# Kernel tuning notes

Hardware: AMD Instinct MI355X
Metric: run time of the kernel (lower is better)

The kernel has to match this reference:

```python
import jax, jax.numpy as jnp
import numpy as np

EPS = 1e-5  # torch LayerNorm default eps
DIM = 2
FEED = 10


def layernorm(x, g, b):
    mu = jnp.mean(x, axis=-1, keepdims=True)
    var = jnp.mean((x - mu) ** 2, axis=-1, keepdims=True)
    return (x - mu) * jax.lax.rsqrt(var + EPS) * g + b


def mha(q, k, v, w_in, b_in, w_out, b_out):
    # nn.MultiheadAttention with n_heads=1: head_dim == embed_dim
    E = q.shape[-1]
    wq, wk, wv = jnp.split(w_in, 3, axis=0)
    bq, bk, bv = jnp.split(b_in, 3)
    qh = q @ wq.T + bq  # [B,Sq,E]
    kh = k @ wk.T + bk  # [B,Sk,E]
    vh = v @ wv.T + bv
    scale = 1.0 / np.sqrt(E).astype(np.float32)
    scores = jnp.einsum('bqd,bkd->bqk', qh, kh) * scale  # [B,Sq,Sk]
    attn = jax.nn.softmax(scores, axis=-1)
    out = jnp.einsum('bqk,bkd->bqd', attn, vh)
    return out @ w_out.T + b_out


def setup_inputs() -> dict:
    key = jax.random.key(0)
    ks = jax.random.split(key, 16)
    d, fd = DIM, FEED
    s = 0.5
    inp = {
        'x': jax.random.normal(ks[0], (32, 32, 256, d), dtype=jnp.float32),
        'm': jax.random.normal(ks[1], (1024, 256, d), dtype=jnp.float32),
        # self-attention params
        'sa_w_in': jax.random.normal(ks[2], (3 * d, d), dtype=jnp.float32) * s,
        'sa_b_in': jnp.zeros((3 * d,), dtype=jnp.float32),
        'sa_w_out': jax.random.normal(ks[3], (d, d), dtype=jnp.float32) * s,
        'sa_b_out': jnp.zeros((d,), dtype=jnp.float32),
        # cross-attention params
        'ca_w_in': jax.random.normal(ks[4], (3 * d, d), dtype=jnp.float32) * s,
        'ca_b_in': jnp.zeros((3 * d,), dtype=jnp.float32),
        'ca_w_out': jax.random.normal(ks[5], (d, d), dtype=jnp.float32) * s,
        'ca_b_out': jnp.zeros((d,), dtype=jnp.float32),
        # layernorms
        'ln1_g': jnp.ones((d,), dtype=jnp.float32),
        'ln1_b': jnp.zeros((d,), dtype=jnp.float32),
        'ln2_g': jnp.ones((d,), dtype=jnp.float32),
        'ln2_b': jnp.zeros((d,), dtype=jnp.float32),
        'ln3_g': jnp.ones((d,), dtype=jnp.float32),
        'ln3_b': jnp.zeros((d,), dtype=jnp.float32),
        # feed-forward: Linear(d,fd) -> LayerNorm(fd) -> ReLU -> Linear(fd,d)
        'f_w1': jax.random.normal(ks[6], (fd, d), dtype=jnp.float32) * s,
        'f_b1': jnp.zeros((fd,), dtype=jnp.float32),
        'f_ln_g': jnp.ones((fd,), dtype=jnp.float32),
        'f_ln_b': jnp.zeros((fd,), dtype=jnp.float32),
        'f_w2': jax.random.normal(ks[7], (d, fd), dtype=jnp.float32) * s,
        'f_b2': jnp.zeros((d,), dtype=jnp.float32),
    }
    return inp


def reference(x, m, sa_w_in, sa_b_in, sa_w_out, sa_b_out,
              ca_w_in, ca_b_in, ca_w_out, ca_b_out,
              ln1_g, ln1_b, ln2_g, ln2_b, ln3_g, ln3_b,
              f_w1, f_b1, f_ln_g, f_ln_b, f_w2, f_b2):
    b, k, s, f = x.shape
    h = x.reshape(-1, s, f)  # [b*k, s, f]
    h = layernorm(h, ln1_g, ln1_b)
    h = h + mha(h, h, h, sa_w_in, sa_b_in, sa_w_out, sa_b_out)
    h = layernorm(h, ln2_g, ln2_b)
    h = h + mha(h, m, m, ca_w_in, ca_b_in, ca_w_out, ca_b_out)
    h = layernorm(h, ln3_g, ln3_b)
    ff = h @ f_w1.T + f_b1
    ff = layernorm(ff, f_ln_g, f_ln_b)
    ff = jax.nn.relu(ff) @ f_w2.T + f_b2
    h = h + ff
    return h.reshape(b, k, s, f)
```

## Files before the change

### kernel.cpp

```cpp
#include <hip/hip_runtime.h>

#define NTOK 256
#define LOG2E 1.44269504088896340736f
#define LN_EPS 1e-5f

__global__ __launch_bounds__(512, 8)
void att_decoder_kernel(
    const float* __restrict__ x, const float* __restrict__ m,
    const float* __restrict__ sa_w_in, const float* __restrict__ sa_b_in,
    const float* __restrict__ sa_w_out, const float* __restrict__ sa_b_out,
    const float* __restrict__ ca_w_in, const float* __restrict__ ca_b_in,
    const float* __restrict__ ca_w_out, const float* __restrict__ ca_b_out,
    const float* __restrict__ ln1_g, const float* __restrict__ ln1_b,
    const float* __restrict__ ln2_g, const float* __restrict__ ln2_b,
    const float* __restrict__ ln3_g, const float* __restrict__ ln3_b,
    const float* __restrict__ f_w1, const float* __restrict__ f_b1,
    const float* __restrict__ f_ln_g, const float* __restrict__ f_ln_b,
    const float* __restrict__ f_w2, const float* __restrict__ f_b2,
    float* __restrict__ out)
{
    const int b   = blockIdx.x;
    const int tid = threadIdx.x;
    const int t   = tid & (NTOK - 1);
    const int kh  = tid >> 8;

    __shared__ float4 kv_s[NTOK];
    __shared__ float4 part_s[512];

    float2 hv = ((const float2*)x)[b * NTOK + t];
    float h0 = hv.x, h1 = hv.y;

    {
        float diff = 0.5f * (h0 - h1);
        float n = diff * rsqrtf(diff * diff + LN_EPS);
        h0 =  n * ln1_g[0] + ln1_b[0];
        h1 = -n * ln1_g[1] + ln1_b[1];
    }

    const float sc = 0.7071067811865476f * LOG2E;

    {
        float q0 = h0*sa_w_in[0] + h1*sa_w_in[1] + sa_b_in[0];
        float q1 = h0*sa_w_in[2] + h1*sa_w_in[3] + sa_b_in[1];
        float qe0 = q0 * sc, qe1 = q1 * sc;
        if (kh == 0) {
            float4 kv;
            kv.x = h0*sa_w_in[4]  + h1*sa_w_in[5]  + sa_b_in[2];
            kv.y = h0*sa_w_in[6]  + h1*sa_w_in[7]  + sa_b_in[3];
            kv.z = h0*sa_w_in[8]  + h1*sa_w_in[9]  + sa_b_in[4];
            kv.w = h0*sa_w_in[10] + h1*sa_w_in[11] + sa_b_in[5];
            kv_s[t] = kv;
        }
        __syncthreads();
        const int kbase = kh * (NTOK / 2);
        float l = 0.f, a0 = 0.f, a1 = 0.f;
        #pragma unroll 8
        for (int k = 0; k < NTOK / 2; ++k) {
            float4 kv = kv_s[kbase + k];
            float s = qe0 * kv.x + qe1 * kv.y;
            float p = __builtin_amdgcn_exp2f(s);
            l  += p;
            a0 += p * kv.z;
            a1 += p * kv.w;
        }
        part_s[tid] = make_float4(l, a0, a1, 0.f);
        __syncthreads();
        float4 o = part_s[tid ^ 256];
        l += o.x; a0 += o.y; a1 += o.z;
        float rl = 1.0f / l;
        a0 *= rl; a1 *= rl;
        h0 += a0*sa_w_out[0] + a1*sa_w_out[1] + sa_b_out[0];
        h1 += a0*sa_w_out[2] + a1*sa_w_out[3] + sa_b_out[1];
    }

    {
        float diff = 0.5f * (h0 - h1);
        float n = diff * rsqrtf(diff * diff + LN_EPS);
        h0 =  n * ln2_g[0] + ln2_b[0];
        h1 = -n * ln2_g[1] + ln2_b[1];
    }

    {
        float q0 = h0*ca_w_in[0] + h1*ca_w_in[1] + ca_b_in[0];
        float q1 = h0*ca_w_in[2] + h1*ca_w_in[3] + ca_b_in[1];
        float qe0 = q0 * sc, qe1 = q1 * sc;
        if (kh == 0) {
            float2 mv = ((const float2*)m)[b * NTOK + t];
            float4 kv;
            kv.x = mv.x*ca_w_in[4]  + mv.y*ca_w_in[5]  + ca_b_in[2];
            kv.y = mv.x*ca_w_in[6]  + mv.y*ca_w_in[7]  + ca_b_in[3];
            kv.z = mv.x*ca_w_in[8]  + mv.y*ca_w_in[9]  + ca_b_in[4];
            kv.w = mv.x*ca_w_in[10] + mv.y*ca_w_in[11] + ca_b_in[5];
            kv_s[t] = kv;
        }
        __syncthreads();
        const int kbase = kh * (NTOK / 2);
        float l = 0.f, a0 = 0.f, a1 = 0.f;
        #pragma unroll 8
        for (int k = 0; k < NTOK / 2; ++k) {
            float4 kv = kv_s[kbase + k];
            float s = qe0 * kv.x + qe1 * kv.y;
            float p = __builtin_amdgcn_exp2f(s);
            l  += p;
            a0 += p * kv.z;
            a1 += p * kv.w;
        }
        part_s[tid] = make_float4(l, a0, a1, 0.f);
        __syncthreads();
        float4 o = part_s[tid ^ 256];
        l += o.x; a0 += o.y; a1 += o.z;
        float rl = 1.0f / l;
        a0 *= rl; a1 *= rl;
        h0 += a0*ca_w_out[0] + a1*ca_w_out[1] + ca_b_out[0];
        h1 += a0*ca_w_out[2] + a1*ca_w_out[3] + ca_b_out[1];
    }

    if (kh != 0) return;

    {
        float diff = 0.5f * (h0 - h1);
        float n = diff * rsqrtf(diff * diff + LN_EPS);
        h0 =  n * ln3_g[0] + ln3_b[0];
        h1 = -n * ln3_g[1] + ln3_b[1];
    }

    {
        float ff[10];
        #pragma unroll
        for (int i = 0; i < 10; ++i)
            ff[i] = h0*f_w1[2*i] + h1*f_w1[2*i+1] + f_b1[i];
        float mu = 0.f;
        #pragma unroll
        for (int i = 0; i < 10; ++i) mu += ff[i];
        mu *= 0.1f;
        float var = 0.f;
        #pragma unroll
        for (int i = 0; i < 10; ++i) { float d = ff[i] - mu; var += d * d; }
        var *= 0.1f;
        float r = rsqrtf(var + LN_EPS);
        float o0 = 0.f, o1 = 0.f;
        #pragma unroll
        for (int i = 0; i < 10; ++i) {
            float n = (ff[i] - mu) * r * f_ln_g[i] + f_ln_b[i];
            n = fmaxf(n, 0.f);
            o0 += n * f_w2[i];
            o1 += n * f_w2[10 + i];
        }
        h0 += o0 + f_b2[0];
        h1 += o1 + f_b2[1];
    }

    ((float2*)out)[b * NTOK + t] = make_float2(h0, h1);
}

extern "C" void kernel_launch(void* const* d_in, const int* in_sizes, int n_in,
                              void* d_out, int out_size, void* d_ws, size_t ws_size,
                              hipStream_t stream) {
    const float* x        = (const float*)d_in[0];
    const float* m        = (const float*)d_in[1];
    const float* sa_w_in  = (const float*)d_in[2];
    const float* sa_b_in  = (const float*)d_in[3];
    const float* sa_w_out = (const float*)d_in[4];
    const float* sa_b_out = (const float*)d_in[5];
    const float* ca_w_in  = (const float*)d_in[6];
    const float* ca_b_in  = (const float*)d_in[7];
    const float* ca_w_out = (const float*)d_in[8];
    const float* ca_b_out = (const float*)d_in[9];
    const float* ln1_g    = (const float*)d_in[10];
    const float* ln1_b    = (const float*)d_in[11];
    const float* ln2_g    = (const float*)d_in[12];
    const float* ln2_b    = (const float*)d_in[13];
    const float* ln3_g    = (const float*)d_in[14];
    const float* ln3_b    = (const float*)d_in[15];
    const float* f_w1     = (const float*)d_in[16];
    const float* f_b1     = (const float*)d_in[17];
    const float* f_ln_g   = (const float*)d_in[18];
    const float* f_ln_b   = (const float*)d_in[19];
    const float* f_w2     = (const float*)d_in[20];
    const float* f_b2     = (const float*)d_in[21];

    const int nbatch = in_sizes[0] / (NTOK * 2);
    att_decoder_kernel<<<nbatch, 512, 0, stream>>>(
        x, m, sa_w_in, sa_b_in, sa_w_out, sa_b_out,
        ca_w_in, ca_b_in, ca_w_out, ca_b_out,
        ln1_g, ln1_b, ln2_g, ln2_b, ln3_g, ln3_b,
        f_w1, f_b1, f_ln_g, f_ln_b, f_w2, f_b2,
        (float*)d_out);
}
```

Baseline: 124.0 us.

## Process two queries per thread with packed float2 math and 4-way key split

Each thread now handles two query tokens (t and t+128) held in 2-wide float vectors, so every shared-memory K/V load is reused for two queries and the packed FMA instructions can be used. Keys are split four ways instead of two, and the partial sums are reduced across four slices. The self-attention and cross-attention K/V tables are built together up front in separate shared buffers, which removes one barrier phase. The cost is more registers per thread, a larger cross-thread reduction, and only 128 threads doing the final feed-forward and store.

```diff
diff --git a/kernel.cpp b/kernel.cpp
--- a/kernel.cpp
+++ b/kernel.cpp
@@ -3,6 +3,10 @@
 #define NTOK 256
 #define LOG2E 1.44269504088896340736f
 #define LN_EPS 1e-5f
+
+typedef float v2f __attribute__((ext_vector_type(2)));
+
+static __device__ __forceinline__ v2f splat(float s) { v2f r; r.x = s; r.y = s; return r; }
 
 __global__ __launch_bounds__(512, 8)
 void att_decoder_kernel(
@@ -19,138 +23,156 @@
     const float* __restrict__ f_w2, const float* __restrict__ f_b2,
     float* __restrict__ out)
 {
-    const int b   = blockIdx.x;
     const int tid = threadIdx.x;
-    const int t   = tid & (NTOK - 1);
-    const int kh  = tid >> 8;
-
-    __shared__ float4 kv_s[NTOK];
-    __shared__ float4 part_s[512];
-
-    float2 hv = ((const float2*)x)[b * NTOK + t];
-    float h0 = hv.x, h1 = hv.y;
-
-    {
-        float diff = 0.5f * (h0 - h1);
-        float n = diff * rsqrtf(diff * diff + LN_EPS);
-        h0 =  n * ln1_g[0] + ln1_b[0];
-        h1 = -n * ln1_g[1] + ln1_b[1];
-    }
-
-    const float sc = 0.7071067811865476f * LOG2E;
-
-    {
-        float q0 = h0*sa_w_in[0] + h1*sa_w_in[1] + sa_b_in[0];
-        float q1 = h0*sa_w_in[2] + h1*sa_w_in[3] + sa_b_in[1];
-        float qe0 = q0 * sc, qe1 = q1 * sc;
-        if (kh == 0) {
+    const int row = blockIdx.x;
+    const int qp  = tid & 127;
+    const int kh  = tid >> 7;
+
+    __shared__ float4 kv_sa[NTOK];
+    __shared__ float4 kv_ca[NTOK];
+    __shared__ v2f    part[3][512];
+
+    const float2* __restrict__ x2 = (const float2*)x;
+    const float2* __restrict__ m2 = (const float2*)m;
+
+    {
+        const int j = tid & 255;
+        if (tid < 256) {
+            float2 xv = x2[row * NTOK + j];
+            float d = 0.5f * (xv.x - xv.y);
+            float n = d * rsqrtf(d * d + LN_EPS);
+            float h0 =  n * ln1_g[0] + ln1_b[0];
+            float h1 = -n * ln1_g[1] + ln1_b[1];
             float4 kv;
             kv.x = h0*sa_w_in[4]  + h1*sa_w_in[5]  + sa_b_in[2];
             kv.y = h0*sa_w_in[6]  + h1*sa_w_in[7]  + sa_b_in[3];
             kv.z = h0*sa_w_in[8]  + h1*sa_w_in[9]  + sa_b_in[4];
             kv.w = h0*sa_w_in[10] + h1*sa_w_in[11] + sa_b_in[5];
-            kv_s[t] = kv;
-        }
-        __syncthreads();
-        const int kbase = kh * (NTOK / 2);
-        float l = 0.f, a0 = 0.f, a1 = 0.f;
-        #pragma unroll 8
-        for (int k = 0; k < NTOK / 2; ++k) {
-            float4 kv = kv_s[kbase + k];
-            float s = qe0 * kv.x + qe1 * kv.y;
-            float p = __builtin_amdgcn_exp2f(s);
-            l  += p;
-            a0 += p * kv.z;
-            a1 += p * kv.w;
-        }
-        part_s[tid] = make_float4(l, a0, a1, 0.f);
-        __syncthreads();
-        float4 o = part_s[tid ^ 256];
-        l += o.x; a0 += o.y; a1 += o.z;
-        float rl = 1.0f / l;
-        a0 *= rl; a1 *= rl;
-        h0 += a0*sa_w_out[0] + a1*sa_w_out[1] + sa_b_out[0];
-        h1 += a0*sa_w_out[2] + a1*sa_w_out[3] + sa_b_out[1];
-    }
-
-    {
-        float diff = 0.5f * (h0 - h1);
-        float n = diff * rsqrtf(diff * diff + LN_EPS);
-        h0 =  n * ln2_g[0] + ln2_b[0];
-        h1 = -n * ln2_g[1] + ln2_b[1];
-    }
-
-    {
-        float q0 = h0*ca_w_in[0] + h1*ca_w_in[1] + ca_b_in[0];
-        float q1 = h0*ca_w_in[2] + h1*ca_w_in[3] + ca_b_in[1];
-        float qe0 = q0 * sc, qe1 = q1 * sc;
-        if (kh == 0) {
-            float2 mv = ((const float2*)m)[b * NTOK + t];
+            kv_sa[j] = kv;
+        } else {
+            float2 mv = m2[row * NTOK + j];
             float4 kv;
             kv.x = mv.x*ca_w_in[4]  + mv.y*ca_w_in[5]  + ca_b_in[2];
             kv.y = mv.x*ca_w_in[6]  + mv.y*ca_w_in[7]  + ca_b_in[3];
             kv.z = mv.x*ca_w_in[8]  + mv.y*ca_w_in[9]  + ca_b_in[4];
             kv.w = mv.x*ca_w_in[10] + mv.y*ca_w_in[11] + ca_b_in[5];
-            kv_s[t] = kv;
-        }
+            kv_ca[j] = kv;
+        }
+    }
+
+    float2 xa = x2[row * NTOK + qp];
+    float2 xb = x2[row * NTOK + qp + 128];
+    v2f h0, h1;
+    {
+        float da = 0.5f * (xa.x - xa.y);
+        float na = da * rsqrtf(da * da + LN_EPS);
+        float db = 0.5f * (xb.x - xb.y);
+        float nb = db * rsqrtf(db * db + LN_EPS);
+        h0.x =  na*ln1_g[0] + ln1_b[0];  h0.y =  nb*ln1_g[0] + ln1_b[0];
+        h1.x = -na*ln1_g[1] + ln1_b[1];  h1.y = -nb*ln1_g[1] + ln1_b[1];
+    }
+
+    __syncthreads();
+
+    const float sc = 0.7071067811865476f * LOG2E;
+    const int kbase = kh * 64;
+
+    {
+        v2f qe0 = (h0*splat(sa_w_in[0]) + h1*splat(sa_w_in[1]) + splat(sa_b_in[0])) * splat(sc);
+        v2f qe1 = (h0*splat(sa_w_in[2]) + h1*splat(sa_w_in[3]) + splat(sa_b_in[1])) * splat(sc);
+        v2f l = splat(0.f), a0 = splat(0.f), a1 = splat(0.f);
+        #pragma unroll 8
+        for (int k = 0; k < 64; ++k) {
+            float4 kv = kv_sa[kbase + k];
+            v2f s = qe0*splat(kv.x) + qe1*splat(kv.y);
+            v2f p; p.x = __builtin_amdgcn_exp2f(s.x);
+                   p.y = __builtin_amdgcn_exp2f(s.y);
+            l += p; a0 += p*splat(kv.z); a1 += p*splat(kv.w);
+        }
+        part[0][tid] = l; part[1][tid] = a0; part[2][tid] = a1;
         __syncthreads();
-        const int kbase = kh * (NTOK / 2);
-        float l = 0.f, a0 = 0.f, a1 = 0.f;
+        v2f L  = part[0][qp] + part[0][qp+128] + part[0][qp+256] + part[0][qp+384];
+        v2f A0 = part[1][qp] + part[1][qp+128] + part[1][qp+256] + part[1][qp+384];
+        v2f A1 = part[2][qp] + part[2][qp+128] + part[2][qp+256] + part[2][qp+384];
+        v2f rl; rl.x = 1.0f / L.x; rl.y = 1.0f / L.y;
+        A0 *= rl; A1 *= rl;
+        h0 += A0*splat(sa_w_out[0]) + A1*splat(sa_w_out[1]) + splat(sa_b_out[0]);
+        h1 += A0*splat(sa_w_out[2]) + A1*splat(sa_w_out[3]) + splat(sa_b_out[1]);
+    }
+
+    {
+        float da = 0.5f * (h0.x - h1.x);
+        float na = da * rsqrtf(da * da + LN_EPS);
+        float db = 0.5f * (h0.y - h1.y);
+        float nb = db * rsqrtf(db * db + LN_EPS);
+        h0.x =  na*ln2_g[0] + ln2_b[0];  h0.y =  nb*ln2_g[0] + ln2_b[0];
+        h1.x = -na*ln2_g[1] + ln2_b[1];  h1.y = -nb*ln2_g[1] + ln2_b[1];
+    }
+
+    __syncthreads();
+
+    {
+        v2f qe0 = (h0*splat(ca_w_in[0]) + h1*splat(ca_w_in[1]) + splat(ca_b_in[0])) * splat(sc);
+        v2f qe1 = (h0*splat(ca_w_in[2]) + h1*splat(ca_w_in[3]) + splat(ca_b_in[1])) * splat(sc);
+        v2f l = splat(0.f), a0 = splat(0.f), a1 = splat(0.f);
         #pragma unroll 8
-        for (int k = 0; k < NTOK / 2; ++k) {
-            float4 kv = kv_s[kbase + k];
-            float s = qe0 * kv.x + qe1 * kv.y;
-            float p = __builtin_amdgcn_exp2f(s);
-            l  += p;
-            a0 += p * kv.z;
-            a1 += p * kv.w;
-        }
-        part_s[tid] = make_float4(l, a0, a1, 0.f);
+        for (int k = 0; k < 64; ++k) {
+            float4 kv = kv_ca[kbase + k];
+            v2f s = qe0*splat(kv.x) + qe1*splat(kv.y);
+            v2f p; p.x = __builtin_amdgcn_exp2f(s.x);
+                   p.y = __builtin_amdgcn_exp2f(s.y);
+            l += p; a0 += p*splat(kv.z); a1 += p*splat(kv.w);
+        }
+        part[0][tid] = l; part[1][tid] = a0; part[2][tid] = a1;
         __syncthreads();
-        float4 o = part_s[tid ^ 256];
-        l += o.x; a0 += o.y; a1 += o.z;
-        float rl = 1.0f / l;
-        a0 *= rl; a1 *= rl;
-        h0 += a0*ca_w_out[0] + a1*ca_w_out[1] + ca_b_out[0];
-        h1 += a0*ca_w_out[2] + a1*ca_w_out[3] + ca_b_out[1];
-    }
-
-    if (kh != 0) return;
-
-    {
-        float diff = 0.5f * (h0 - h1);
-        float n = diff * rsqrtf(diff * diff + LN_EPS);
-        h0 =  n * ln3_g[0] + ln3_b[0];
-        h1 = -n * ln3_g[1] + ln3_b[1];
-    }
-
-    {
-        float ff[10];
+        if (tid >= 128) return;
+        v2f L  = part[0][qp] + part[0][qp+128] + part[0][qp+256] + part[0][qp+384];
+        v2f A0 = part[1][qp] + part[1][qp+128] + part[1][qp+256] + part[1][qp+384];
+        v2f A1 = part[2][qp] + part[2][qp+128] + part[2][qp+256] + part[2][qp+384];
+        v2f rl; rl.x = 1.0f / L.x; rl.y = 1.0f / L.y;
+        A0 *= rl; A1 *= rl;
+        h0 += A0*splat(ca_w_out[0]) + A1*splat(ca_w_out[1]) + splat(ca_b_out[0]);
+        h1 += A0*splat(ca_w_out[2]) + A1*splat(ca_w_out[3]) + splat(ca_b_out[1]);
+    }
+
+    {
+        float da = 0.5f * (h0.x - h1.x);
+        float na = da * rsqrtf(da * da + LN_EPS);
+        float db = 0.5f * (h0.y - h1.y);
+        float nb = db * rsqrtf(db * db + LN_EPS);
+        h0.x =  na*ln3_g[0] + ln3_b[0];  h0.y =  nb*ln3_g[0] + ln3_b[0];
+        h1.x = -na*ln3_g[1] + ln3_b[1];  h1.y = -nb*ln3_g[1] + ln3_b[1];
+    }
+
+    {
+        v2f ff[10];
         #pragma unroll
         for (int i = 0; i < 10; ++i)
-            ff[i] = h0*f_w1[2*i] + h1*f_w1[2*i+1] + f_b1[i];
-        float mu = 0.f;
+            ff[i] = h0*splat(f_w1[2*i]) + h1*splat(f_w1[2*i+1]) + splat(f_b1[i]);
+        v2f mu = splat(0.f);
         #pragma unroll
         for (int i = 0; i < 10; ++i) mu += ff[i];
-        mu *= 0.1f;
-        float var = 0.f;
-        #pragma unroll
-        for (int i = 0; i < 10; ++i) { float d = ff[i] - mu; var += d * d; }
-        var *= 0.1f;
-        float r = rsqrtf(var + LN_EPS);
-        float o0 = 0.f, o1 = 0.f;
+        mu *= splat(0.1f);
+        v2f var = splat(0.f);
+        #pragma unroll
+        for (int i = 0; i < 10; ++i) { v2f d = ff[i] - mu; var += d * d; }
+        var *= splat(0.1f);
+        v2f r; r.x = rsqrtf(var.x + LN_EPS); r.y = rsqrtf(var.y + LN_EPS);
+        v2f o0 = splat(0.f), o1 = splat(0.f);
         #pragma unroll
         for (int i = 0; i < 10; ++i) {
-            float n = (ff[i] - mu) * r * f_ln_g[i] + f_ln_b[i];
-            n = fmaxf(n, 0.f);
-            o0 += n * f_w2[i];
-            o1 += n * f_w2[10 + i];
-        }
-        h0 += o0 + f_b2[0];
-        h1 += o1 + f_b2[1];
-    }
-
-    ((float2*)out)[b * NTOK + t] = make_float2(h0, h1);
+            v2f n = (ff[i] - mu) * r * splat(f_ln_g[i]) + splat(f_ln_b[i]);
+            n.x = fmaxf(n.x, 0.f); n.y = fmaxf(n.y, 0.f);
+            o0 += n * splat(f_w2[i]);
+            o1 += n * splat(f_w2[10 + i]);
+        }
+        h0 += o0 + splat(f_b2[0]);
+        h1 += o1 + splat(f_b2[1]);
+    }
+
+    float2* out2 = (float2*)out;
+    out2[row * NTOK + qp]       = make_float2(h0.x, h1.x);
+    out2[row * NTOK + qp + 128] = make_float2(h0.y, h1.y);
 }
 
 extern "C" void kernel_launch(void* const* d_in, const int* in_sizes, int n_in,
```

Result: no change. 122.8 us (-1.0%).

## Register-tile 4 queries per thread with DPP quad reductions over key slots

Applied to the files above, without the earlier changes.

Rewrites the attention work split so each thread of a 256-thread block owns 4 queries and a quarter of the keys (strided by 4). Each key/value read from shared memory is reused across 4 queries, and partial softmax sums are combined with DPP quad shuffles instead of a shared-memory exchange and extra barrier. Both self- and cross-attention K/V are precomputed up front behind a single barrier. In exchange there is more register pressure and redundant per-lane final work selected via sel4, plus halved block size.

```diff
diff --git a/kernel.cpp b/kernel.cpp
--- a/kernel.cpp
+++ b/kernel.cpp
@@ -4,7 +4,33 @@
 #define LOG2E 1.44269504088896340736f
 #define LN_EPS 1e-5f
 
-__global__ __launch_bounds__(512, 8)
+typedef float v4f __attribute__((ext_vector_type(4)));
+
+static __device__ __forceinline__ v4f splat4(float s) {
+    v4f r; r.x = s; r.y = s; r.z = s; r.w = s; return r;
+}
+
+template <int CTRL>
+static __device__ __forceinline__ float dppq(float v) {
+    return __int_as_float(
+        __builtin_amdgcn_update_dpp(0, __float_as_int(v), CTRL, 0xF, 0xF, true));
+}
+static __device__ __forceinline__ v4f quad_sum(v4f v) {
+    v4f t;
+    t.x = dppq<0xB1>(v.x); t.y = dppq<0xB1>(v.y);
+    t.z = dppq<0xB1>(v.z); t.w = dppq<0xB1>(v.w);
+    v += t;
+    t.x = dppq<0x4E>(v.x); t.y = dppq<0x4E>(v.y);
+    t.z = dppq<0x4E>(v.z); t.w = dppq<0x4E>(v.w);
+    return v + t;
+}
+static __device__ __forceinline__ float sel4(v4f v, int kq) {
+    float ab = (kq & 1) ? v.y : v.x;
+    float cd = (kq & 1) ? v.w : v.z;
+    return (kq & 2) ? cd : ab;
+}
+
+__global__ __launch_bounds__(256, 8)
 void att_decoder_kernel(
     const float* __restrict__ x, const float* __restrict__ m,
     const float* __restrict__ sa_w_in, const float* __restrict__ sa_b_in,
@@ -19,116 +45,130 @@
     const float* __restrict__ f_w2, const float* __restrict__ f_b2,
     float* __restrict__ out)
 {
-    const int b   = blockIdx.x;
-    const int tid = threadIdx.x;
-    const int t   = tid & (NTOK - 1);
-    const int kh  = tid >> 8;
-
-    __shared__ float4 kv_s[NTOK];
-    __shared__ float4 part_s[512];
-
-    float2 hv = ((const float2*)x)[b * NTOK + t];
-    float h0 = hv.x, h1 = hv.y;
-
-    {
-        float diff = 0.5f * (h0 - h1);
-        float n = diff * rsqrtf(diff * diff + LN_EPS);
-        h0 =  n * ln1_g[0] + ln1_b[0];
-        h1 = -n * ln1_g[1] + ln1_b[1];
-    }
+    const int tid  = threadIdx.x;
+    const int row  = blockIdx.x;
+    const int lane = tid & 63;
+    const int w    = tid >> 6;
+    const int kq   = lane & 3;
+    const int qg   = (w << 4) + (lane >> 2);
+
+    __shared__ float4 kv_sa[NTOK];
+    __shared__ float4 kv_ca[NTOK];
+
+    const float2* __restrict__ x2 = (const float2*)x;
+    const float2* __restrict__ m2 = (const float2*)m;
+
+    {
+        const int j = (tid >> 2) | ((tid & 3) << 6);
+        float2 xv = x2[row * NTOK + j];
+        float d = 0.5f * (xv.x - xv.y);
+        float n = d * rsqrtf(d * d + LN_EPS);
+        float h0 =  n * ln1_g[0] + ln1_b[0];
+        float h1 = -n * ln1_g[1] + ln1_b[1];
+        float4 kv;
+        kv.x = h0*sa_w_in[4]  + h1*sa_w_in[5]  + sa_b_in[2];
+        kv.y = h0*sa_w_in[6]  + h1*sa_w_in[7]  + sa_b_in[3];
+        kv.z = h0*sa_w_in[8]  + h1*sa_w_in[9]  + sa_b_in[4];
+        kv.w = h0*sa_w_in[10] + h1*sa_w_in[11] + sa_b_in[5];
+        kv_sa[tid] = kv;
+        float2 mv = m2[row * NTOK + j];
+        kv.x = mv.x*ca_w_in[4]  + mv.y*ca_w_in[5]  + ca_b_in[2];
+        kv.y = mv.x*ca_w_in[6]  + mv.y*ca_w_in[7]  + ca_b_in[3];
+        kv.z = mv.x*ca_w_in[8]  + mv.y*ca_w_in[9]  + ca_b_in[4];
+        kv.w = mv.x*ca_w_in[10] + mv.y*ca_w_in[11] + ca_b_in[5];
+        kv_ca[tid] = kv;
+    }
+
+    v4f h0, h1;
+    {
+        float2 q0 = x2[row * NTOK + qg];
+        float2 q1 = x2[row * NTOK + qg + 64];
+        float2 q2 = x2[row * NTOK + qg + 128];
+        float2 q3 = x2[row * NTOK + qg + 192];
+        const float g0 = ln1_g[0], b0 = ln1_b[0], g1 = ln1_g[1], b1 = ln1_b[1];
+#define LN1C(QV, C) { float d_ = 0.5f*(QV.x - QV.y);                       \
+        float n_ = d_ * rsqrtf(d_*d_ + LN_EPS);                             \
+        h0.C = n_*g0 + b0; h1.C = -n_*g1 + b1; }
+        LN1C(q0, x) LN1C(q1, y) LN1C(q2, z) LN1C(q3, w)
+#undef LN1C
+    }
+
+    __syncthreads();
 
     const float sc = 0.7071067811865476f * LOG2E;
-
-    {
-        float q0 = h0*sa_w_in[0] + h1*sa_w_in[1] + sa_b_in[0];
-        float q1 = h0*sa_w_in[2] + h1*sa_w_in[3] + sa_b_in[1];
-        float qe0 = q0 * sc, qe1 = q1 * sc;
-        if (kh == 0) {
-            float4 kv;
-            kv.x = h0*sa_w_in[4]  + h1*sa_w_in[5]  + sa_b_in[2];
-            kv.y = h0*sa_w_in[6]  + h1*sa_w_in[7]  + sa_b_in[3];
-            kv.z = h0*sa_w_in[8]  + h1*sa_w_in[9]  + sa_b_in[4];
-            kv.w = h0*sa_w_in[10] + h1*sa_w_in[11] + sa_b_in[5];
-            kv_s[t] = kv;
+    const int slot0 = kq;
+
+    {
+        v4f qe0 = (h0*splat4(sa_w_in[0]) + h1*splat4(sa_w_in[1]) + splat4(sa_b_in[0])) * splat4(sc);
+        v4f qe1 = (h0*splat4(sa_w_in[2]) + h1*splat4(sa_w_in[3]) + splat4(sa_b_in[1])) * splat4(sc);
+        v4f l = splat4(0.f), a0 = splat4(0.f), a1 = splat4(0.f);
+        #pragma unroll 8
+        for (int i = 0; i < 64; ++i) {
+            float4 kv = kv_sa[(i << 2) + slot0];
+            v4f s = qe0*splat4(kv.x) + qe1*splat4(kv.y);
+            v4f p;
+            p.x = __builtin_amdgcn_exp2f(s.x);
+            p.y = __builtin_amdgcn_exp2f(s.y);
+            p.z = __builtin_amdgcn_exp2f(s.z);
+            p.w = __builtin_amdgcn_exp2f(s.w);
+            l += p; a0 += p*splat4(kv.z); a1 += p*splat4(kv.w);
         }
-        __syncthreads();
-        const int kbase = kh * (NTOK / 2);
-        float l = 0.f, a0 = 0.f, a1 = 0.f;
+        l = quad_sum(l); a0 = quad_sum(a0); a1 = quad_sum(a1);
+        v4f rl;
+        rl.x = 1.0f/l.x; rl.y = 1.0f/l.y; rl.z = 1.0f/l.z; rl.w = 1.0f/l.w;
+        a0 *= rl; a1 *= rl;
+        h0 += a0*splat4(sa_w_out[0]) + a1*splat4(sa_w_out[1]) + splat4(sa_b_out[0]);
+        h1 += a0*splat4(sa_w_out[2]) + a1*splat4(sa_w_out[3]) + splat4(sa_b_out[1]);
+    }
+
+    {
+        const float g0 = ln2_g[0], b0 = ln2_b[0], g1 = ln2_g[1], b1 = ln2_b[1];
+#define LN2C(C) { float d_ = 0.5f*(h0.C - h1.C);                           \
+        float n_ = d_ * rsqrtf(d_*d_ + LN_EPS);                             \
+        h0.C = n_*g0 + b0; h1.C = -n_*g1 + b1; }
+        LN2C(x) LN2C(y) LN2C(z) LN2C(w)
+#undef LN2C
+    }
+
+    v4f cl, ca0, ca1;
+    {
+        v4f qe0 = (h0*splat4(ca_w_in[0]) + h1*splat4(ca_w_in[1]) + splat4(ca_b_in[0])) * splat4(sc);
+        v4f qe1 = (h0*splat4(ca_w_in[2]) + h1*splat4(ca_w_in[3]) + splat4(ca_b_in[1])) * splat4(sc);
+        v4f l = splat4(0.f), a0 = splat4(0.f), a1 = splat4(0.f);
         #pragma unroll 8
-        for (int k = 0; k < NTOK / 2; ++k) {
-            float4 kv = kv_s[kbase + k];
-            float s = qe0 * kv.x + qe1 * kv.y;
-            float p = __builtin_amdgcn_exp2f(s);
-            l  += p;
-            a0 += p * kv.z;
-            a1 += p * kv.w;
+        for (int i = 0; i < 64; ++i) {
+            float4 kv = kv_ca[(i << 2) + slot0];
+            v4f s = qe0*splat4(kv.x) + qe1*splat4(kv.y);
+            v4f p;
+            p.x = __builtin_amdgcn_exp2f(s.x);
+            p.y = __builtin_amdgcn_exp2f(s.y);
+            p.z = __builtin_amdgcn_exp2f(s.z);
+            p.w = __builtin_amdgcn_exp2f(s.w);
+            l += p; a0 += p*splat4(kv.z); a1 += p*splat4(kv.w);
         }
-        part_s[tid] = make_float4(l, a0, a1, 0.f);
-        __syncthreads();
-        float4 o = part_s[tid ^ 256];
-        l += o.x; a0 += o.y; a1 += o.z;
-        float rl = 1.0f / l;
-        a0 *= rl; a1 *= rl;
-        h0 += a0*sa_w_out[0] + a1*sa_w_out[1] + sa_b_out[0];
-        h1 += a0*sa_w_out[2] + a1*sa_w_out[3] + sa_b_out[1];
-    }
-
-    {
-        float diff = 0.5f * (h0 - h1);
-        float n = diff * rsqrtf(diff * diff + LN_EPS);
-        h0 =  n * ln2_g[0] + ln2_b[0];
-        h1 = -n * ln2_g[1] + ln2_b[1];
-    }
-
-    {
-        float q0 = h0*ca_w_in[0] + h1*ca_w_in[1] + ca_b_in[0];
-        float q1 = h0*ca_w_in[2] + h1*ca_w_in[3] + ca_b_in[1];
-        float qe0 = q0 * sc, qe1 = q1 * sc;
-        if (kh == 0) {
-            float2 mv = ((const float2*)m)[b * NTOK + t];
-            float4 kv;
-            kv.x = mv.x*ca_w_in[4]  + mv.y*ca_w_in[5]  + ca_b_in[2];
-            kv.y = mv.x*ca_w_in[6]  + mv.y*ca_w_in[7]  + ca_b_in[3];
-            kv.z = mv.x*ca_w_in[8]  + mv.y*ca_w_in[9]  + ca_b_in[4];
-            kv.w = mv.x*ca_w_in[10] + mv.y*ca_w_in[11] + ca_b_in[5];
-            kv_s[t] = kv;
-        }
-        __syncthreads();
-        const int kbase = kh * (NTOK / 2);
-        float l = 0.f, a0 = 0.f, a1 = 0.f;
-        #pragma unroll 8
-        for (int k = 0; k < NTOK / 2; ++k) {
-            float4 kv = kv_s[kbase + k];
-            float s = qe0 * kv.x + qe1 * kv.y;
-            float p = __builtin_amdgcn_exp2f(s);
-            l  += p;
-            a0 += p * kv.z;
-            a1 += p * kv.w;
-        }
-        part_s[tid] = make_float4(l, a0, a1, 0.f);
-        __syncthreads();
-        float4 o = part_s[tid ^ 256];
-        l += o.x; a0 += o.y; a1 += o.z;
-        float rl = 1.0f / l;
-        a0 *= rl; a1 *= rl;
-        h0 += a0*ca_w_out[0] + a1*ca_w_out[1] + ca_b_out[0];
-        h1 += a0*ca_w_out[2] + a1*ca_w_out[3] + ca_b_out[1];
-    }
-
-    if (kh != 0) return;
-
-    {
-        float diff = 0.5f * (h0 - h1);
-        float n = diff * rsqrtf(diff * diff + LN_EPS);
-        h0 =  n * ln3_g[0] + ln3_b[0];
-        h1 = -n * ln3_g[1] + ln3_b[1];
+        cl = quad_sum(l); ca0 = quad_sum(a0); ca1 = quad_sum(a1);
+    }
+
+    float L   = sel4(cl, kq);
+    float A0  = sel4(ca0, kq) / L;
+    float A1  = sel4(ca1, kq) / L;
+    float s0  = sel4(h0, kq);
+    float s1  = sel4(h1, kq);
+    s0 += A0*ca_w_out[0] + A1*ca_w_out[1] + ca_b_out[0];
+    s1 += A0*ca_w_out[2] + A1*ca_w_out[3] + ca_b_out[1];
+
+    {
+        float d = 0.5f*(s0 - s1);
+        float n = d * rsqrtf(d*d + LN_EPS);
+        s0 =  n*ln3_g[0] + ln3_b[0];
+        s1 = -n*ln3_g[1] + ln3_b[1];
     }
 
     {
         float ff[10];
         #pragma unroll
         for (int i = 0; i < 10; ++i)
-            ff[i] = h0*f_w1[2*i] + h1*f_w1[2*i+1] + f_b1[i];
+            ff[i] = s0*f_w1[2*i] + s1*f_w1[2*i+1] + f_b1[i];
         float mu = 0.f;
         #pragma unroll
         for (int i = 0; i < 10; ++i) mu += ff[i];
@@ -146,11 +186,11 @@
             o0 += n * f_w2[i];
             o1 += n * f_w2[10 + i];
         }
-        h0 += o0 + f_b2[0];
-        h1 += o1 + f_b2[1];
-    }
-
-    ((float2*)out)[b * NTOK + t] = make_float2(h0, h1);
+        s0 += o0 + f_b2[0];
+        s1 += o1 + f_b2[1];
+    }
+
+    ((float2*)out)[row * NTOK + qg + (kq << 6)] = make_float2(s0, s1);
 }
 
 extern "C" void kernel_launch(void* const* d_in, const int* in_sizes, int n_in,
@@ -180,7 +220,7 @@
     const float* f_b2     = (const float*)d_in[21];
 
     const int nbatch = in_sizes[0] / (NTOK * 2);
-    att_decoder_kernel<<<nbatch, 512, 0, stream>>>(
+    att_decoder_kernel<<<nbatch, 256, 0, stream>>>(
         x, m, sa_w_in, sa_b_in, sa_w_out, sa_b_out,
         ca_w_in, ca_b_in, ca_w_out, ca_b_out,
         ln1_g, ln1_b, ln2_g, ln2_b, ln3_g, ln3_b,
```

Result: no change. 123.4 us (-0.5%).
